# Performance work log

Measured on AMD Instinct MI355X. Metric: run time of the kernel, lower is better.

## Reference

```python
import jax, jax.numpy as jnp
import numpy as np

BN_EPS = 1e-5
NUM_PROPOSALS = 200
NUM_CLASSES = 10

def _conv2d(x, w, pad):
    return jax.lax.conv_general_dilated(
        x, w, window_strides=(1, 1), padding=((pad, pad), (pad, pad)),
        dimension_numbers=("NCHW", "OIHW", "NCHW"))

def setup_inputs() -> dict:
    key = jax.random.key(0)
    ks = jax.random.split(key, 6)
    B, C, H, W = 4, 256, 180, 180
    # bev_pos = create_2D_grid(H, W): grid centers, shape [1, H*W, 2]
    gx, gy = jnp.meshgrid(jnp.linspace(0.0, H - 1.0, H), jnp.linspace(0.0, W - 1.0, W), indexing="ij")
    bev_pos = jnp.stack([gx + 0.5, gy + 0.5], axis=0).reshape(1, 2, -1).transpose(0, 2, 1)
    return {
        "bev_feats": jax.random.normal(ks[0], (B, C, H, W), jnp.float32),
        "bev_pos": bev_pos.astype(jnp.float32),
        "conv1_w": jax.random.normal(ks[1], (C, C, 3, 3), jnp.float32) * 0.02,
        "bn_gamma": jnp.ones((C,), jnp.float32),
        "bn_beta": jnp.zeros((C,), jnp.float32),
        "bn_mean": jnp.zeros((C,), jnp.float32),
        "bn_var": jnp.ones((C,), jnp.float32),
        "conv2_w": jax.random.normal(ks[2], (NUM_CLASSES, C, 3, 3), jnp.float32) * 0.02,
        "conv2_b": jnp.zeros((NUM_CLASSES,), jnp.float32),
        "ce_w": jax.random.normal(ks[3], (C, NUM_CLASSES, 1), jnp.float32) * 0.1,
        "ce_b": jnp.zeros((C,), jnp.float32),
    }

def reference(bev_feats, bev_pos, conv1_w, bn_gamma, bn_beta, bn_mean, bn_var, conv2_w, conv2_b, ce_w, ce_b):
    B, C, H, W = bev_feats.shape
    HW = H * W
    bev_flat = bev_feats.reshape(B, C, HW)  # [B, C, HW]

    # heatmap head: Conv3x3 (no bias) -> BN (running stats) -> ReLU -> Conv3x3 + bias
    x = _conv2d(bev_feats, conv1_w, pad=1)
    x = (x - bn_mean[None, :, None, None]) * (bn_gamma / jnp.sqrt(bn_var + BN_EPS))[None, :, None, None] + bn_beta[None, :, None, None]
    x = jax.nn.relu(x)
    dense_heatmap = _conv2d(x, conv2_w, pad=1) + conv2_b[None, :, None, None]  # [B, 10, H, W]

    heatmap = jax.nn.sigmoid(jax.lax.stop_gradient(dense_heatmap))
    # NMS-style local max: 3x3 max pool (stride 1, VALID), placed into zero-padded borders
    inner = jax.lax.reduce_window(heatmap, -jnp.inf, jax.lax.max,
                                  (1, 1, 3, 3), (1, 1, 1, 1), "VALID")
    local_max = jnp.zeros_like(heatmap).at[:, :, 1:-1, 1:-1].set(inner)
    # nuScenes: pedestrian (8) and traffic cone (9) use kernel-1 pooling (identity)
    local_max = local_max.at[:, 8].set(heatmap[:, 8]).at[:, 9].set(heatmap[:, 9])
    heatmap = heatmap * (heatmap == local_max)
    heatmap_flat = heatmap.reshape(B, NUM_CLASSES, HW)

    # global top-k over classes x positions
    _, top = jax.lax.top_k(heatmap_flat.reshape(B, -1), NUM_PROPOSALS)  # [B, P]
    query_labels = top // HW                                            # [B, P]
    pos_idx = top % HW                                                  # [B, P]

    query_pos = jnp.take(bev_pos[0], pos_idx, axis=0)                   # [B, P, 2]
    query_feat = jnp.take_along_axis(bev_flat, pos_idx[:, None, :], axis=2)  # [B, C, P]
    one_hot = jax.nn.one_hot(query_labels, NUM_CLASSES, dtype=jnp.float32).transpose(0, 2, 1)  # [B, 10, P]
    query_feat = query_feat + jnp.einsum("ok,bkp->bop", ce_w[:, :, 0], one_hot) + ce_b[None, :, None]
    query_heatmap_score = jnp.take_along_axis(heatmap_flat, jnp.broadcast_to(pos_idx[:, None, :], (B, NUM_CLASSES, NUM_PROPOSALS)), axis=2)
    return query_feat, query_pos, query_labels, query_heatmap_score, dense_heatmap
```

## Files before the change

### kernel.cpp

```cpp
#include <hip/hip_runtime.h>
#include <hip/hip_bf16.h>
#include <stdint.h>

#define H 180
#define W 180
#define HW 32400
#define CIN 256
#define NCLS 10
#define NPROP 200
#define WTAP 589824
#define WTAP2 36864

#define OFF_X      0ULL
#define OFF_NMS    0ULL
#define OFF_HIST   5184000ULL
#define OFF_CNT    5249536ULL
#define OFF_CAND   5249568ULL
#define OFF_BSEL   5380640ULL
#define OFF_TPOS   5380672ULL
#define OFF_TLAB   5383872ULL

typedef __attribute__((ext_vector_type(8))) short short8;
typedef __attribute__((ext_vector_type(4))) float f32x4;

__device__ __forceinline__ float sigm(float v) { return 1.0f / (1.0f + expf(-v)); }

__device__ __forceinline__ unsigned bfround(unsigned u) {
    return (u + 0x7FFFu + ((u >> 16) & 1u)) >> 16;
}
__device__ __forceinline__ void splitbf(float v, short &hi, short &lo) {
    unsigned u = __float_as_uint(v);
    unsigned hb = bfround(u);
    float fh = __uint_as_float(hb << 16);
    unsigned lb = bfround(__float_as_uint(v - fh));
    hi = (short)hb; lo = (short)lb;
}

__global__ void split_w_kernel(const float* __restrict__ w1, short* __restrict__ Wq)
{
    int idx = blockIdx.x * 256 + threadIdx.x;
    if (idx >= WTAP) return;
    int e = idx & 7, co = (idx >> 3) & 255, cig = (idx >> 11) & 31, tap = idx >> 16;
    int ci = cig * 8 + e;
    float v = w1[((size_t)co * CIN + ci) * 9 + tap];
    short h, l; splitbf(v, h, l);
    Wq[idx] = h; Wq[WTAP + idx] = l;
}

__global__ void split_w2_kernel(const float* __restrict__ w2, short* __restrict__ Wq2)
{
    int idx = blockIdx.x * 256 + threadIdx.x;
    if (idx >= WTAP2) return;
    int e = idx & 7, co = (idx >> 3) & 15, cig = (idx >> 7) & 31, tap = idx >> 12;
    int ci = cig * 8 + e;
    float v = (co < NCLS) ? w2[((size_t)co * CIN + ci) * 9 + tap] : 0.f;
    short h, l; splitbf(v, h, l);
    Wq2[idx] = h; Wq2[WTAP2 + idx] = l;
}

__global__ __launch_bounds__(256, 2)
void conv1_mfma(const float* __restrict__ in, const short* __restrict__ Wq,
                const float* __restrict__ gamma, const float* __restrict__ beta,
                const float* __restrict__ mean, const float* __restrict__ var,
                float* __restrict__ xout)
{
    __shared__ short Xs[2][2][6][34][36];
    const int b    = blockIdx.z >> 1;
    const int co0  = (blockIdx.z & 1) * 128;
    const int y0   = blockIdx.y * 4;
    const int col0 = blockIdx.x * 32;
    const int tid  = threadIdx.x;
    const int w    = tid >> 6;
    const int lane = tid & 63;
    const int li = lane & 15, lg = lane >> 4;
    const int cobase = co0 + w * 32;

    f32x4 acc[2][4][2];
    #pragma unroll
    for (int ct = 0; ct < 2; ++ct)
        #pragma unroll
        for (int r = 0; r < 4; ++r)
            #pragma unroll
            for (int c = 0; c < 2; ++c) acc[ct][r][c] = (f32x4){0.f,0.f,0.f,0.f};

    int sl_[4], rr_[4], cc_[4];
    bool va_[4], inb_[4];
    const float* src_[4];
    #pragma unroll
    for (int it = 0; it < 4; ++it) {
        int is = tid + it * 256;
        bool va = is < 816;
        int isc = va ? is : 0;
        int sl = isc / 204, rem = isc % 204;
        int r = rem / 34, c = rem % 34;
        int gy = y0 - 1 + r, gx = col0 - 1 + c;
        bool inb = va && ((unsigned)gy < (unsigned)H) && ((unsigned)gx < (unsigned)W);
        sl_[it]=sl; rr_[it]=r; cc_[it]=c; va_[it]=va; inb_[it]=inb;
        src_[it] = in + ((size_t)(b*CIN + sl*8) * H + gy) * W + gx;
    }

    float sA[4][8];
    #pragma unroll
    for (int it = 0; it < 4; ++it)
        #pragma unroll
        for (int e = 0; e < 8; ++e)
            sA[it][e] = inb_[it] ? src_[it][(size_t)e * HW] : 0.f;
    #pragma unroll
    for (int it = 0; it < 4; ++it) {
        if (va_[it]) {
            short h[8], l[8];
            #pragma unroll
            for (int e = 0; e < 8; ++e) splitbf(sA[it][e], h[e], l[e]);
            short8 vh, vl;
            #pragma unroll
            for (int e = 0; e < 8; ++e) { vh[e] = h[e]; vl[e] = l[e]; }
            *(short8*)&Xs[0][0][rr_[it]][cc_[it]][sl_[it]*8] = vh;
            *(short8*)&Xs[0][1][rr_[it]][cc_[it]][sl_[it]*8] = vl;
        }
    }
    __syncthreads();

    for (int kc = 0; kc < 8; ++kc) {
        const int cur = kc & 1, nxt = cur ^ 1;
        const bool more = (kc < 7);
        if (more) {
            const size_t coff = (size_t)(kc + 1) * 32 * HW;
            #pragma unroll
            for (int it = 0; it < 4; ++it)
                #pragma unroll
                for (int e = 0; e < 8; ++e)
                    sA[it][e] = inb_[it] ? src_[it][coff + (size_t)e * HW] : 0.f;
        }
        const int cig = kc * 4 + lg;
        const short* pA = Wq + ((size_t)cig * 256 + cobase + li) * 8;
        #pragma unroll
        for (int dx = 0; dx < 3; ++dx) {
            short8 a_h[3][2], a_l[3][2];
            #pragma unroll
            for (int dy = 0; dy < 3; ++dy) {
                const int off = (dy*3 + dx) * 65536;
                a_h[dy][0] = *(const short8*)(pA + off);
                a_h[dy][1] = *(const short8*)(pA + off + 128);
                a_l[dy][0] = *(const short8*)(pA + WTAP + off);
                a_l[dy][1] = *(const short8*)(pA + WTAP + off + 128);
            }
            #pragma unroll
            for (int c16 = 0; c16 < 2; ++c16) {
                const int ccol = c16 * 16 + li + dx;
                short8 bh[6], bl[6];
                #pragma unroll
                for (int rr = 0; rr < 6; ++rr) {
                    bh[rr] = *(const short8*)&Xs[cur][0][rr][ccol][lg*8];
                    bl[rr] = *(const short8*)&Xs[cur][1][rr][ccol][lg*8];
                }
                #pragma unroll
                for (int dy = 0; dy < 3; ++dy) {
                    #pragma unroll
                    for (int r = 0; r < 4; ++r) {
                        #pragma unroll
                        for (int ct = 0; ct < 2; ++ct) {
                            f32x4 a = acc[ct][r][c16];
                            a = __builtin_amdgcn_mfma_f32_16x16x32_bf16(a_h[dy][ct], bh[r+dy], a, 0, 0, 0);
                            a = __builtin_amdgcn_mfma_f32_16x16x32_bf16(a_h[dy][ct], bl[r+dy], a, 0, 0, 0);
                            a = __builtin_amdgcn_mfma_f32_16x16x32_bf16(a_l[dy][ct], bh[r+dy], a, 0, 0, 0);
                            acc[ct][r][c16] = a;
                        }
                    }
                }
            }
        }
        if (more) {
            #pragma unroll
            for (int it = 0; it < 4; ++it) {
                if (va_[it]) {
                    short h[8], l[8];
                    #pragma unroll
                    for (int e = 0; e < 8; ++e) splitbf(sA[it][e], h[e], l[e]);
                    short8 vh, vl;
                    #pragma unroll
                    for (int e = 0; e < 8; ++e) { vh[e] = h[e]; vl[e] = l[e]; }
                    *(short8*)&Xs[nxt][0][rr_[it]][cc_[it]][sl_[it]*8] = vh;
                    *(short8*)&Xs[nxt][1][rr_[it]][cc_[it]][sl_[it]*8] = vl;
                }
            }
        }
        __syncthreads();
    }

    #pragma unroll
    for (int ct = 0; ct < 2; ++ct) {
        float scv[4], shv[4];
        #pragma unroll
        for (int q = 0; q < 4; ++q) {
            int co = cobase + ct*16 + lg*4 + q;
            float s = gamma[co] / sqrtf(var[co] + 1e-5f);
            scv[q] = s; shv[q] = beta[co] - mean[co] * s;
        }
        #pragma unroll
        for (int r = 0; r < 4; ++r) {
            #pragma unroll
            for (int c16 = 0; c16 < 2; ++c16) {
                int x = col0 + c16*16 + li;
                if (x < W) {
                    #pragma unroll
                    for (int q = 0; q < 4; ++q) {
                        int co = cobase + ct*16 + lg*4 + q;
                        float v = fmaxf(fmaf(acc[ct][r][c16][q], scv[q], shv[q]), 0.f);
                        xout[((size_t)(b*CIN + co) * H + (y0 + r)) * W + x] = v;
                    }
                }
            }
        }
    }
}

__global__ __launch_bounds__(256, 2)
void conv2_mfma(const float* __restrict__ x, const short* __restrict__ Wq2,
                const float* __restrict__ bias, float* __restrict__ dense)
{
    __shared__ short Xs[2][2][6][34][36];
    const int b    = blockIdx.z;
    const int y0   = blockIdx.y * 4;
    const int col0 = blockIdx.x * 32;
    const int tid  = threadIdx.x;
    const int w    = tid >> 6;
    const int lane = tid & 63;
    const int li = lane & 15, lg = lane >> 4;
    const int c16w = w & 1, rh = w >> 1;

    f32x4 acc2[2];
    acc2[0] = (f32x4){0.f,0.f,0.f,0.f};
    acc2[1] = (f32x4){0.f,0.f,0.f,0.f};

    int sl_[4], rr_[4], cc_[4];
    bool va_[4], inb_[4];
    const float* src_[4];
    #pragma unroll
    for (int it = 0; it < 4; ++it) {
        int is = tid + it * 256;
        bool va = is < 816;
        int isc = va ? is : 0;
        int sl = isc / 204, rem = isc % 204;
        int r = rem / 34, c = rem % 34;
        int gy = y0 - 1 + r, gx = col0 - 1 + c;
        bool inb = va && ((unsigned)gy < (unsigned)H) && ((unsigned)gx < (unsigned)W);
        sl_[it]=sl; rr_[it]=r; cc_[it]=c; va_[it]=va; inb_[it]=inb;
        src_[it] = x + ((size_t)(b*CIN + sl*8) * H + gy) * W + gx;
    }

    float sA[4][8];
    #pragma unroll
    for (int it = 0; it < 4; ++it)
        #pragma unroll
        for (int e = 0; e < 8; ++e)
            sA[it][e] = inb_[it] ? src_[it][(size_t)e * HW] : 0.f;
    #pragma unroll
    for (int it = 0; it < 4; ++it) {
        if (va_[it]) {
            short h[8], l[8];
            #pragma unroll
            for (int e = 0; e < 8; ++e) splitbf(sA[it][e], h[e], l[e]);
            short8 vh, vl;
            #pragma unroll
            for (int e = 0; e < 8; ++e) { vh[e] = h[e]; vl[e] = l[e]; }
            *(short8*)&Xs[0][0][rr_[it]][cc_[it]][sl_[it]*8] = vh;
            *(short8*)&Xs[0][1][rr_[it]][cc_[it]][sl_[it]*8] = vl;
        }
    }
    __syncthreads();

    for (int kc = 0; kc < 8; ++kc) {
        const int cur = kc & 1, nxt = cur ^ 1;
        const bool more = (kc < 7);
        if (more) {
            const size_t coff = (size_t)(kc + 1) * 32 * HW;
            #pragma unroll
            for (int it = 0; it < 4; ++it)
                #pragma unroll
                for (int e = 0; e < 8; ++e)
                    sA[it][e] = inb_[it] ? src_[it][coff + (size_t)e * HW] : 0.f;
        }
        const int cig = kc * 4 + lg;
        const short* pA = Wq2 + ((size_t)cig * 16 + li) * 8;
        #pragma unroll
        for (int dx = 0; dx < 3; ++dx) {
            short8 a_h[3], a_l[3];
            #pragma unroll
            for (int dy = 0; dy < 3; ++dy) {
                const int off = (dy*3 + dx) * 4096;
                a_h[dy] = *(const short8*)(pA + off);
                a_l[dy] = *(const short8*)(pA + WTAP2 + off);
            }
            const int ccol = c16w * 16 + li + dx;
            short8 bh[4], bl[4];
            #pragma unroll
            for (int rr = 0; rr < 4; ++rr) {
                bh[rr] = *(const short8*)&Xs[cur][0][rh*2 + rr][ccol][lg*8];
                bl[rr] = *(const short8*)&Xs[cur][1][rh*2 + rr][ccol][lg*8];
            }
            #pragma unroll
            for (int dy = 0; dy < 3; ++dy) {
                #pragma unroll
                for (int r2 = 0; r2 < 2; ++r2) {
                    f32x4 a = acc2[r2];
                    a = __builtin_amdgcn_mfma_f32_16x16x32_bf16(a_h[dy], bh[r2+dy], a, 0, 0, 0);
                    a = __builtin_amdgcn_mfma_f32_16x16x32_bf16(a_h[dy], bl[r2+dy], a, 0, 0, 0);
                    a = __builtin_amdgcn_mfma_f32_16x16x32_bf16(a_l[dy], bh[r2+dy], a, 0, 0, 0);
                    acc2[r2] = a;
                }
            }
        }
        if (more) {
            #pragma unroll
            for (int it = 0; it < 4; ++it) {
                if (va_[it]) {
                    short h[8], l[8];
                    #pragma unroll
                    for (int e = 0; e < 8; ++e) splitbf(sA[it][e], h[e], l[e]);
                    short8 vh, vl;
                    #pragma unroll
                    for (int e = 0; e < 8; ++e) { vh[e] = h[e]; vl[e] = l[e]; }
                    *(short8*)&Xs[nxt][0][rr_[it]][cc_[it]][sl_[it]*8] = vh;
                    *(short8*)&Xs[nxt][1][rr_[it]][cc_[it]][sl_[it]*8] = vl;
                }
            }
        }
        __syncthreads();
    }

    #pragma unroll
    for (int r2 = 0; r2 < 2; ++r2) {
        const int y = y0 + rh*2 + r2;
        const int xc = col0 + c16w*16 + li;
        if (xc < W) {
            #pragma unroll
            for (int q = 0; q < 4; ++q) {
                int co = lg*4 + q;
                if (co < NCLS)
                    dense[((size_t)(b*NCLS + co) * H + y) * W + xc] = acc2[r2][q] + bias[co];
            }
        }
    }
}

__global__ void nms_kernel(const float* __restrict__ dense, float* __restrict__ nms)
{
    const int x = threadIdx.x;
    if (x >= W) return;
    const int bk = blockIdx.x;
    const int y = blockIdx.y;
    const int k = bk % NCLS;
    const float* p = dense + (size_t)bk * HW;
    float c = sigm(p[y*W + x]);
    float outv;
    if (k >= 8) {
        outv = c;
    } else if (x == 0 || x == W-1 || y == 0 || y == H-1) {
        outv = 0.f;
    } else {
        float m = c;
        #pragma unroll
        for (int dy = -1; dy <= 1; ++dy)
            #pragma unroll
            for (int dx = -1; dx <= 1; ++dx) {
                if (dy == 0 && dx == 0) continue;
                m = fmaxf(m, sigm(p[(y+dy)*W + (x+dx)]));
            }
        outv = (c == m) ? c : 0.f;
    }
    nms[(size_t)bk * HW + y*W + x] = outv;
}

__global__ void hist_kernel(const float* __restrict__ nms, int* __restrict__ hist)
{
    __shared__ int h[4096];
    const int b = blockIdx.y;
    for (int l = threadIdx.x; l < 4096; l += 256) h[l] = 0;
    __syncthreads();
    const float* p = nms + (size_t)b * (NCLS*HW);
    for (int i = blockIdx.x*256 + threadIdx.x; i < NCLS*HW; i += gridDim.x*256) {
        float v = p[i];
        if (v > 0.f) {
            int bin = (int)(v * 4096.f);
            if (bin > 4095) bin = 4095;
            atomicAdd(&h[bin], 1);
        }
    }
    __syncthreads();
    for (int l = threadIdx.x; l < 4096; l += 256)
        if (h[l]) atomicAdd(&hist[b*4096 + l], h[l]);
}

__global__ void scan_kernel(const int* __restrict__ hist, int* __restrict__ bsel)
{
    __shared__ int ss[256];
    const int b = blockIdx.x;
    const int t = threadIdx.x;
    const int base = 4096 - 16*(t+1);
    int s = 0;
    #pragma unroll
    for (int i = 0; i < 16; ++i) s += hist[b*4096 + base + i];
    ss[t] = s;
    __syncthreads();
    for (int off = 1; off < 256; off <<= 1) {
        int v = (t >= off) ? ss[t-off] : 0;
        __syncthreads();
        ss[t] += v;
        __syncthreads();
    }
    int incl = ss[t];
    int excl = incl - s;
    if (excl < NPROP && incl >= NPROP) {
        int acc2 = excl, bfound = base;
        for (int bin = base + 15; bin >= base; --bin) {
            acc2 += hist[b*4096 + bin];
            if (acc2 >= NPROP) { bfound = bin; break; }
        }
        bsel[b] = bfound;
    }
    if (t == 255 && ss[255] < NPROP) bsel[b] = 0;
}

__global__ void collect_kernel(const float* __restrict__ nms, const int* __restrict__ bsel,
                               int* __restrict__ cnt, unsigned long long* __restrict__ cand)
{
    const int b = blockIdx.y;
    const int B0 = bsel[b];
    const float* p = nms + (size_t)b * (NCLS*HW);
    for (int i = blockIdx.x*256 + threadIdx.x; i < NCLS*HW; i += gridDim.x*256) {
        float v = p[i];
        if (v > 0.f) {
            int bin = (int)(v * 4096.f);
            if (bin > 4095) bin = 4095;
            if (bin >= B0) {
                int slot = atomicAdd(&cnt[b], 1);
                if (slot < 4096) {
                    unsigned int vb = __float_as_uint(v);
                    cand[(size_t)b*4096 + slot] =
                        ((unsigned long long)(~vb) << 32) | (unsigned int)i;
                }
            }
        }
    }
}

__global__ void sort_emit(const unsigned long long* __restrict__ cand, const int* __restrict__ cnt,
                          const float* __restrict__ nms, const float* __restrict__ bev_pos,
                          float* __restrict__ out, int* __restrict__ tpos, int* __restrict__ tlab)
{
    __shared__ unsigned long long key[4096];
    const int b = blockIdx.x;
    const int t = threadIdx.x;
    int n = cnt[b]; if (n > 4096) n = 4096;
    for (int l = t; l < 4096; l += 1024)
        key[l] = (l < n) ? cand[(size_t)b*4096 + l] : ~0ULL;
    __syncthreads();
    for (int k = 2; k <= 4096; k <<= 1) {
        for (int jj = k >> 1; jj > 0; jj >>= 1) {
            for (int l = t; l < 2048; l += 1024) {
                int i  = 2*l - (l & (jj-1));
                int ix = i + jj;
                bool up = ((i & k) == 0);
                unsigned long long a = key[i], c = key[ix];
                if ((a > c) == up) { key[i] = c; key[ix] = a; }
            }
            __syncthreads();
        }
    }
    for (int p = t; p < NPROP; p += 1024) {
        unsigned long long kk = key[p];
        unsigned int idx = (unsigned int)kk;
        if (idx >= (unsigned)(NCLS*HW)) idx = 0;
        int label = idx / HW;
        int pos   = idx % HW;
        out[206400 + b*NPROP + p] = (float)label;
        out[204800 + (b*NPROP + p)*2 + 0] = bev_pos[pos*2 + 0];
        out[204800 + (b*NPROP + p)*2 + 1] = bev_pos[pos*2 + 1];
        tpos[b*NPROP + p] = pos;
        tlab[b*NPROP + p] = label;
        #pragma unroll
        for (int k2 = 0; k2 < NCLS; ++k2)
            out[207200 + (b*NCLS + k2)*NPROP + p] = nms[((size_t)b*NCLS + k2)*HW + pos];
    }
}

__global__ void feat_kernel(const float* __restrict__ bev, const float* __restrict__ cew,
                            const float* __restrict__ ceb, const int* __restrict__ tpos,
                            const int* __restrict__ tlab, float* __restrict__ out)
{
    const int c = blockIdx.x, b = blockIdx.y;
    const int t = threadIdx.x;
    if (t >= NPROP) return;
    int pos = tpos[b*NPROP + t];
    int lab = tlab[b*NPROP + t];
    float v = bev[((size_t)b*CIN + c)*HW + pos] + cew[c*NCLS + lab] + ceb[c];
    out[((size_t)b*CIN + c)*NPROP + t] = v;
}

extern "C" void kernel_launch(void* const* d_in, const int* in_sizes, int n_in,
                              void* d_out, int out_size, void* d_ws, size_t ws_size,
                              hipStream_t stream)
{
    const float* bev   = (const float*)d_in[0];
    const float* bpos  = (const float*)d_in[1];
    const float* w1    = (const float*)d_in[2];
    const float* gamma = (const float*)d_in[3];
    const float* beta  = (const float*)d_in[4];
    const float* mean  = (const float*)d_in[5];
    const float* var   = (const float*)d_in[6];
    const float* w2    = (const float*)d_in[7];
    const float* b2    = (const float*)d_in[8];
    const float* cew   = (const float*)d_in[9];
    const float* ceb   = (const float*)d_in[10];
    float* out = (float*)d_out;
    char* ws = (char*)d_ws;

    float* xbuf = (float*)(ws + OFF_X);
    float* nmsb = (float*)(ws + OFF_NMS);
    int* hist   = (int*)(ws + OFF_HIST);
    int* cnt    = (int*)(ws + OFF_CNT);
    unsigned long long* cand = (unsigned long long*)(ws + OFF_CAND);
    int* bsel   = (int*)(ws + OFF_BSEL);
    int* tpos   = (int*)(ws + OFF_TPOS);
    int* tlab   = (int*)(ws + OFF_TLAB);
    float* dense = out + 215200;
    short* Wq  = (short*)(out + 215200);
    short* Wq2 = (short*)out;

    split_w_kernel <<<(WTAP  + 255)/256, 256, 0, stream>>>(w1, Wq);
    split_w2_kernel<<<(WTAP2 + 255)/256, 256, 0, stream>>>(w2, Wq2);
    conv1_mfma<<<dim3(6, 45, 8), 256, 0, stream>>>(bev, Wq, gamma, beta, mean, var, xbuf);
    conv2_mfma<<<dim3(6, 45, 4), 256, 0, stream>>>(xbuf, Wq2, b2, dense);
    hipMemsetAsync(ws + OFF_HIST, 0, 65536 + 32, stream);
    nms_kernel  <<<dim3(40, 180),   192, 0, stream>>>(dense, nmsb);
    hist_kernel <<<dim3(32, 4),     256, 0, stream>>>(nmsb, hist);
    scan_kernel <<<4,               256, 0, stream>>>(hist, bsel);
    collect_kernel<<<dim3(64, 4),   256, 0, stream>>>(nmsb, bsel, cnt, cand);
    sort_emit   <<<4,              1024, 0, stream>>>(cand, cnt, nmsb, bpos, out, tpos, tlab);
    feat_kernel <<<dim3(256, 4),    256, 0, stream>>>(bev, cew, ceb, tpos, tlab, out);
}
```

Before: 778.8 us.

## Switch conv1 to 32x32x16 MFMA with single LDS buffer and shrink top-k sort

Conv1 is rewritten to use 32x32x16 bf16 MFMA tiles, where each wave covers 32 output channels by 32 columns per row. The weight layout is repacked to match, and the LDS double buffer is collapsed to a single buffer with an extra barrier. Launch bounds are raised to target 3 blocks per CU, aiming at better occupancy and fewer MFMA issues. Separately, the candidate buffer and bitonic sort shrink from 4096 to 2048 entries, which cuts sort work but risks dropping candidates if more than 2048 pass the histogram threshold.

```diff
diff --git a/kernel.cpp b/kernel.cpp
--- a/kernel.cpp
+++ b/kernel.cpp
@@ -22,6 +22,7 @@
 
 typedef __attribute__((ext_vector_type(8))) short short8;
 typedef __attribute__((ext_vector_type(4))) float f32x4;
+typedef __attribute__((ext_vector_type(16))) float f32x16;
 
 __device__ __forceinline__ float sigm(float v) { return 1.0f / (1.0f + expf(-v)); }
 
@@ -40,11 +41,11 @@
 {
     int idx = blockIdx.x * 256 + threadIdx.x;
     if (idx >= WTAP) return;
-    int e = idx & 7, co = (idx >> 3) & 255, cig = (idx >> 11) & 31, tap = idx >> 16;
-    int ci = cig * 8 + e;
+    int e = idx & 7, h = (idx >> 3) & 1, co = (idx >> 4) & 255, g = (idx >> 12) & 15, tap = idx >> 16;
+    int ci = g * 16 + h * 8 + e;
     float v = w1[((size_t)co * CIN + ci) * 9 + tap];
-    short h, l; splitbf(v, h, l);
-    Wq[idx] = h; Wq[WTAP + idx] = l;
+    short hh, ll; splitbf(v, hh, ll);
+    Wq[idx] = hh; Wq[WTAP + idx] = ll;
 }
 
 __global__ void split_w2_kernel(const float* __restrict__ w2, short* __restrict__ Wq2)
@@ -58,13 +59,13 @@
     Wq2[idx] = h; Wq2[WTAP2 + idx] = l;
 }
 
-__global__ __launch_bounds__(256, 2)
+__global__ __launch_bounds__(256, 3)
 void conv1_mfma(const float* __restrict__ in, const short* __restrict__ Wq,
                 const float* __restrict__ gamma, const float* __restrict__ beta,
                 const float* __restrict__ mean, const float* __restrict__ var,
                 float* __restrict__ xout)
 {
-    __shared__ short Xs[2][2][6][34][36];
+    __shared__ short Xs[2][6][34][36];
     const int b    = blockIdx.z >> 1;
     const int co0  = (blockIdx.z & 1) * 128;
     const int y0   = blockIdx.y * 4;
@@ -72,16 +73,14 @@
     const int tid  = threadIdx.x;
     const int w    = tid >> 6;
     const int lane = tid & 63;
-    const int li = lane & 15, lg = lane >> 4;
+    const int lc = lane & 31, hf = lane >> 5;
     const int cobase = co0 + w * 32;
 
-    f32x4 acc[2][4][2];
-    #pragma unroll
-    for (int ct = 0; ct < 2; ++ct)
-        #pragma unroll
-        for (int r = 0; r < 4; ++r)
-            #pragma unroll
-            for (int c = 0; c < 2; ++c) acc[ct][r][c] = (f32x4){0.f,0.f,0.f,0.f};
+    f32x16 acc[4];
+    #pragma unroll
+    for (int r = 0; r < 4; ++r)
+        #pragma unroll
+        for (int q = 0; q < 16; ++q) acc[r][q] = 0.f;
 
     int sl_[4], rr_[4], cc_[4];
     bool va_[4], inb_[4];
@@ -108,20 +107,25 @@
     #pragma unroll
     for (int it = 0; it < 4; ++it) {
         if (va_[it]) {
-            short h[8], l[8];
-            #pragma unroll
-            for (int e = 0; e < 8; ++e) splitbf(sA[it][e], h[e], l[e]);
+            short h8[8], l8[8];
+            #pragma unroll
+            for (int e = 0; e < 8; ++e) splitbf(sA[it][e], h8[e], l8[e]);
             short8 vh, vl;
             #pragma unroll
-            for (int e = 0; e < 8; ++e) { vh[e] = h[e]; vl[e] = l[e]; }
-            *(short8*)&Xs[0][0][rr_[it]][cc_[it]][sl_[it]*8] = vh;
-            *(short8*)&Xs[0][1][rr_[it]][cc_[it]][sl_[it]*8] = vl;
+            for (int e = 0; e < 8; ++e) { vh[e] = h8[e]; vl[e] = l8[e]; }
+            *(short8*)&Xs[0][rr_[it]][cc_[it]][sl_[it]*8] = vh;
+            *(short8*)&Xs[1][rr_[it]][cc_[it]][sl_[it]*8] = vl;
         }
     }
     __syncthreads();
 
+#define TRI(R, AH, AL, BH, BL) { f32x16 a_ = acc[R]; \
+    a_ = __builtin_amdgcn_mfma_f32_32x32x16_bf16(AH, BH, a_, 0, 0, 0); \
+    a_ = __builtin_amdgcn_mfma_f32_32x32x16_bf16(AH, BL, a_, 0, 0, 0); \
+    a_ = __builtin_amdgcn_mfma_f32_32x32x16_bf16(AL, BH, a_, 0, 0, 0); \
+    acc[R] = a_; }
+
     for (int kc = 0; kc < 8; ++kc) {
-        const int cur = kc & 1, nxt = cur ^ 1;
         const bool more = (kc < 7);
         if (more) {
             const size_t coff = (size_t)(kc + 1) * 32 * HW;
@@ -131,84 +135,83 @@
                 for (int e = 0; e < 8; ++e)
                     sA[it][e] = inb_[it] ? src_[it][coff + (size_t)e * HW] : 0.f;
         }
-        const int cig = kc * 4 + lg;
-        const short* pA = Wq + ((size_t)cig * 256 + cobase + li) * 8;
-        #pragma unroll
-        for (int dx = 0; dx < 3; ++dx) {
-            short8 a_h[3][2], a_l[3][2];
-            #pragma unroll
-            for (int dy = 0; dy < 3; ++dy) {
-                const int off = (dy*3 + dx) * 65536;
-                a_h[dy][0] = *(const short8*)(pA + off);
-                a_h[dy][1] = *(const short8*)(pA + off + 128);
-                a_l[dy][0] = *(const short8*)(pA + WTAP + off);
-                a_l[dy][1] = *(const short8*)(pA + WTAP + off + 128);
-            }
-            #pragma unroll
-            for (int c16 = 0; c16 < 2; ++c16) {
-                const int ccol = c16 * 16 + li + dx;
-                short8 bh[6], bl[6];
-                #pragma unroll
-                for (int rr = 0; rr < 6; ++rr) {
-                    bh[rr] = *(const short8*)&Xs[cur][0][rr][ccol][lg*8];
-                    bl[rr] = *(const short8*)&Xs[cur][1][rr][ccol][lg*8];
-                }
+        #pragma unroll
+        for (int s = 0; s < 2; ++s) {
+            const int g = kc * 2 + s;
+            const int ko = s * 16 + hf * 8;
+            #pragma unroll
+            for (int dx = 0; dx < 3; ++dx) {
+                short8 ah[3], al[3];
                 #pragma unroll
                 for (int dy = 0; dy < 3; ++dy) {
-                    #pragma unroll
-                    for (int r = 0; r < 4; ++r) {
-                        #pragma unroll
-                        for (int ct = 0; ct < 2; ++ct) {
-                            f32x4 a = acc[ct][r][c16];
-                            a = __builtin_amdgcn_mfma_f32_16x16x32_bf16(a_h[dy][ct], bh[r+dy], a, 0, 0, 0);
-                            a = __builtin_amdgcn_mfma_f32_16x16x32_bf16(a_h[dy][ct], bl[r+dy], a, 0, 0, 0);
-                            a = __builtin_amdgcn_mfma_f32_16x16x32_bf16(a_l[dy][ct], bh[r+dy], a, 0, 0, 0);
-                            acc[ct][r][c16] = a;
-                        }
-                    }
+                    const size_t off = (((size_t)(dy*3 + dx)*16 + g)*256 + cobase + lc)*16 + hf*8;
+                    ah[dy] = *(const short8*)(Wq + off);
+                    al[dy] = *(const short8*)(Wq + WTAP + off);
                 }
-            }
-        }
+                const int cc = lc + dx;
+                short8 w0h = *(const short8*)&Xs[0][0][cc][ko];
+                short8 w0l = *(const short8*)&Xs[1][0][cc][ko];
+                short8 w1h = *(const short8*)&Xs[0][1][cc][ko];
+                short8 w1l = *(const short8*)&Xs[1][1][cc][ko];
+                short8 w2h = *(const short8*)&Xs[0][2][cc][ko];
+                short8 w2l = *(const short8*)&Xs[1][2][cc][ko];
+                TRI(0, ah[0], al[0], w0h, w0l);
+                TRI(0, ah[1], al[1], w1h, w1l);
+                TRI(0, ah[2], al[2], w2h, w2l);
+                w0h = *(const short8*)&Xs[0][3][cc][ko];
+                w0l = *(const short8*)&Xs[1][3][cc][ko];
+                TRI(1, ah[0], al[0], w1h, w1l);
+                TRI(1, ah[1], al[1], w2h, w2l);
+                TRI(1, ah[2], al[2], w0h, w0l);
+                w1h = *(const short8*)&Xs[0][4][cc][ko];
+                w1l = *(const short8*)&Xs[1][4][cc][ko];
+                TRI(2, ah[0], al[0], w2h, w2l);
+                TRI(2, ah[1], al[1], w0h, w0l);
+                TRI(2, ah[2], al[2], w1h, w1l);
+                w2h = *(const short8*)&Xs[0][5][cc][ko];
+                w2l = *(const short8*)&Xs[1][5][cc][ko];
+                TRI(3, ah[0], al[0], w0h, w0l);
+                TRI(3, ah[1], al[1], w1h, w1l);
+                TRI(3, ah[2], al[2], w2h, w2l);
+            }
+        }
+        __syncthreads();
         if (more) {
             #pragma unroll
             for (int it = 0; it < 4; ++it) {
                 if (va_[it]) {
-                    short h[8], l[8];
+                    short h8[8], l8[8];
                     #pragma unroll
-                    for (int e = 0; e < 8; ++e) splitbf(sA[it][e], h[e], l[e]);
+                    for (int e = 0; e < 8; ++e) splitbf(sA[it][e], h8[e], l8[e]);
                     short8 vh, vl;
                     #pragma unroll
-                    for (int e = 0; e < 8; ++e) { vh[e] = h[e]; vl[e] = l[e]; }
-                    *(short8*)&Xs[nxt][0][rr_[it]][cc_[it]][sl_[it]*8] = vh;
-                    *(short8*)&Xs[nxt][1][rr_[it]][cc_[it]][sl_[it]*8] = vl;
+                    for (int e = 0; e < 8; ++e) { vh[e] = h8[e]; vl[e] = l8[e]; }
+                    *(short8*)&Xs[0][rr_[it]][cc_[it]][sl_[it]*8] = vh;
+                    *(short8*)&Xs[1][rr_[it]][cc_[it]][sl_[it]*8] = vl;
                 }
             }
         }
         __syncthreads();
     }
-
-    #pragma unroll
-    for (int ct = 0; ct < 2; ++ct) {
-        float scv[4], shv[4];
-        #pragma unroll
-        for (int q = 0; q < 4; ++q) {
-            int co = cobase + ct*16 + lg*4 + q;
-            float s = gamma[co] / sqrtf(var[co] + 1e-5f);
-            scv[q] = s; shv[q] = beta[co] - mean[co] * s;
-        }
+#undef TRI
+
+    float scv[16], shv[16];
+    #pragma unroll
+    for (int q = 0; q < 16; ++q) {
+        int co = cobase + (q & 3) + 8 * (q >> 2) + 4 * hf;
+        float s = gamma[co] / sqrtf(var[co] + 1e-5f);
+        scv[q] = s; shv[q] = beta[co] - mean[co] * s;
+    }
+    const int x = col0 + lc;
+    if (x < W) {
         #pragma unroll
         for (int r = 0; r < 4; ++r) {
-            #pragma unroll
-            for (int c16 = 0; c16 < 2; ++c16) {
-                int x = col0 + c16*16 + li;
-                if (x < W) {
-                    #pragma unroll
-                    for (int q = 0; q < 4; ++q) {
-                        int co = cobase + ct*16 + lg*4 + q;
-                        float v = fmaxf(fmaf(acc[ct][r][c16][q], scv[q], shv[q]), 0.f);
-                        xout[((size_t)(b*CIN + co) * H + (y0 + r)) * W + x] = v;
-                    }
-                }
+            const int y = y0 + r;
+            #pragma unroll
+            for (int q = 0; q < 16; ++q) {
+                int co = cobase + (q & 3) + 8 * (q >> 2) + 4 * hf;
+                float v = fmaxf(fmaf(acc[r][q], scv[q], shv[q]), 0.f);
+                xout[((size_t)(b*CIN + co) * H + y) * W + x] = v;
             }
         }
     }
@@ -434,9 +437,9 @@
             if (bin > 4095) bin = 4095;
             if (bin >= B0) {
                 int slot = atomicAdd(&cnt[b], 1);
-                if (slot < 4096) {
+                if (slot < 2048) {
                     unsigned int vb = __float_as_uint(v);
-                    cand[(size_t)b*4096 + slot] =
+                    cand[(size_t)b*2048 + slot] =
                         ((unsigned long long)(~vb) << 32) | (unsigned int)i;
                 }
             }
@@ -448,22 +451,20 @@
                           const float* __restrict__ nms, const float* __restrict__ bev_pos,
                           float* __restrict__ out, int* __restrict__ tpos, int* __restrict__ tlab)
 {
-    __shared__ unsigned long long key[4096];
+    __shared__ unsigned long long key[2048];
     const int b = blockIdx.x;
     const int t = threadIdx.x;
-    int n = cnt[b]; if (n > 4096) n = 4096;
-    for (int l = t; l < 4096; l += 1024)
-        key[l] = (l < n) ? cand[(size_t)b*4096 + l] : ~0ULL;
+    int n = cnt[b]; if (n > 2048) n = 2048;
+    for (int l = t; l < 2048; l += 1024)
+        key[l] = (l < n) ? cand[(size_t)b*2048 + l] : ~0ULL;
     __syncthreads();
-    for (int k = 2; k <= 4096; k <<= 1) {
+    for (int k = 2; k <= 2048; k <<= 1) {
         for (int jj = k >> 1; jj > 0; jj >>= 1) {
-            for (int l = t; l < 2048; l += 1024) {
-                int i  = 2*l - (l & (jj-1));
-                int ix = i + jj;
-                bool up = ((i & k) == 0);
-                unsigned long long a = key[i], c = key[ix];
-                if ((a > c) == up) { key[i] = c; key[ix] = a; }
-            }
+            int i  = 2*t - (t & (jj-1));
+            int ix = i + jj;
+            bool up = ((i & k) == 0);
+            unsigned long long a = key[i], c = key[ix];
+            if ((a > c) == up) { key[i] = c; key[ix] = a; }
             __syncthreads();
         }
     }
```

Result: slower. 824.2 us (+5.8%).
